# Optimization experiments

Measured on AMD Instinct MI355X. Metric: run time of the kernel, lower is better.

Reference implementation:

```python
import jax, jax.numpy as jnp
import numpy as np

B, S, H = 16, 512, 2048
NH, NKV = 16, 4
HD = H // NH  # 128


def _rope_tables(seq_len, dim, dtype):
    inv_freq = 1.0 / (10000.0 ** (jnp.arange(0, dim, 2, dtype=jnp.float32) / dim))
    t = jnp.arange(seq_len, dtype=jnp.float32)
    freqs = jnp.einsum('i,j->ij', t, inv_freq)          # [S, HD/2]
    emb = jnp.concatenate([freqs, freqs], axis=-1)       # [S, HD]
    cos = jnp.cos(emb)[None, None].astype(dtype)         # [1,1,S,HD]
    sin = jnp.sin(emb)[None, None].astype(dtype)
    return cos, sin


def _rotate_half(x):
    x1, x2 = jnp.split(x, 2, axis=-1)
    return jnp.concatenate([-x2, x1], axis=-1)


def setup_inputs() -> dict:
    key = jax.random.key(0)
    kx, kq, kk, kv, ko = jax.random.split(key, 5)
    x = jax.random.normal(kx, (B, S, H), dtype=jnp.float32)
    s = 0.02
    Wq = jax.random.normal(kq, (H, H), dtype=jnp.float32) * s
    Wk = jax.random.normal(kk, (NKV * HD, H), dtype=jnp.float32) * s
    Wv = jax.random.normal(kv, (NKV * HD, H), dtype=jnp.float32) * s
    Wo = jax.random.normal(ko, (H, H), dtype=jnp.float32) * s
    return {"x": x, "Wq": Wq, "Wk": Wk, "Wv": Wv, "Wo": Wo}


def reference(x, Wq, Wk, Wv, Wo):
    b, s, _ = x.shape
    scaling = HD ** -0.5
    # projections (torch Linear: y = x @ W.T, W is [out,in])
    q = jnp.einsum('bsh,oh->bso', x, Wq).reshape(b, s, NH, HD).transpose(0, 2, 1, 3)
    k = jnp.einsum('bsh,oh->bso', x, Wk).reshape(b, s, NKV, HD).transpose(0, 2, 1, 3)
    v = jnp.einsum('bsh,oh->bso', x, Wv).reshape(b, s, NKV, HD).transpose(0, 2, 1, 3)
    cos, sin = _rope_tables(s, HD, x.dtype)
    q = q * cos + _rotate_half(q) * sin
    k = k * cos + _rotate_half(k) * sin
    rep = NH // NKV
    k = jnp.repeat(k, rep, axis=1)  # [b, NH, s, HD]
    v = jnp.repeat(v, rep, axis=1)
    scores = jnp.einsum('bhqd,bhkd->bhqk', q, k) * scaling
    attn = jax.nn.softmax(scores, axis=-1)
    out = jnp.einsum('bhqk,bhkd->bhqd', attn, v)
    out = out.transpose(0, 2, 1, 3).reshape(b, s, H)
    return jnp.einsum('bsh,oh->bso', out, Wo)
```

## Files before the change

### kernel.cpp

```cpp
#include <hip/hip_runtime.h>
#include <stdint.h>


typedef _Float16 f16;
typedef _Float16 f16x4 __attribute__((ext_vector_type(4)));
typedef _Float16 f16x8 __attribute__((ext_vector_type(8)));
typedef float f32x4 __attribute__((ext_vector_type(4)));

#define B_   16
#define S_   512
#define H_   2048
#define NH_  16
#define NKV_ 4
#define HD_  128
#define ATT_SCALE 0.08838834764831843f
#define LOG2_10000_DIV64 0.20762050593045952f

#define AS1 __attribute__((address_space(1)))
#define AS3 __attribute__((address_space(3)))

__device__ __forceinline__ void async16(const void* g, const void* l) {
  __builtin_amdgcn_global_load_lds((const AS1 unsigned int*)(uintptr_t)g,
                                   (AS3 unsigned int*)(uintptr_t)l, 16, 0, 0);
}

__global__ __launch_bounds__(256) void cast_f32_f16(const float* __restrict__ src,
                                                    f16* __restrict__ dst, int n4) {
  int i = blockIdx.x * 256 + threadIdx.x;
  if (i < n4) {
    float4 v = reinterpret_cast<const float4*>(src)[i];
    f16x4 o = {(f16)v.x, (f16)v.y, (f16)v.z, (f16)v.w};
    reinterpret_cast<f16x4*>(dst)[i] = o;
  }
}

__global__ __launch_bounds__(256) void gemm_qkv(const f16* __restrict__ A,
                                                const f16* __restrict__ W,
                                                f16* __restrict__ qo,
                                                f16* __restrict__ ko,
                                                f16* __restrict__ vto) {
  __shared__ __align__(16) f16 As[128 * 32];
  __shared__ __align__(16) f16 Bs[128 * 32];
  const int K = 2048;
  const int m0 = blockIdx.x * 128;
  const int n0 = blockIdx.y * 128;
  const int tid = threadIdx.x;
  const int wave = tid >> 6, lane = tid & 63;
  const int quad = lane >> 4, l15 = lane & 15;
  const int c0 = wave * 128 + lane;
  const int row0 = c0 >> 2, kc0 = c0 & 3;
  const int row1 = (c0 + 64) >> 2, kc1 = (c0 + 64) & 3;

  f32x4 acc[2][8] = {};

  for (int k0 = 0; k0 < K; k0 += 32) {
    async16(A + (size_t)(m0 + row0) * K + k0 + kc0 * 8, (const char*)As + (wave * 128) * 16);
    async16(A + (size_t)(m0 + row1) * K + k0 + kc1 * 8, (const char*)As + (wave * 128 + 64) * 16);
    async16(W + (size_t)(n0 + row0) * K + k0 + kc0 * 8, (const char*)Bs + (wave * 128) * 16);
    async16(W + (size_t)(n0 + row1) * K + k0 + kc1 * 8, (const char*)Bs + (wave * 128 + 64) * 16);
    __syncthreads();
    f16x8 a[2], b[8];
#pragma unroll
    for (int mi = 0; mi < 2; ++mi)
      a[mi] = *reinterpret_cast<const f16x8*>(As + (wave * 32 + mi * 16 + l15) * 32 + quad * 8);
#pragma unroll
    for (int ni = 0; ni < 8; ++ni)
      b[ni] = *reinterpret_cast<const f16x8*>(Bs + (ni * 16 + l15) * 32 + quad * 8);
#pragma unroll
    for (int mi = 0; mi < 2; ++mi)
#pragma unroll
      for (int ni = 0; ni < 8; ++ni)
        acc[mi][ni] = __builtin_amdgcn_mfma_f32_16x16x32_f16(a[mi], b[ni], acc[mi][ni], 0, 0, 0);
    __syncthreads();
  }

  const int b_ = m0 >> 9;
  if (n0 >= 2560) {
    const int h = (n0 - 2560) >> 7;
    f16* vb = vto + ((size_t)b_ * NKV_ + h) * HD_ * S_;
#pragma unroll
    for (int mi = 0; mi < 2; ++mi)
#pragma unroll
      for (int r = 0; r < 4; ++r) {
        const int s = (m0 + wave * 32 + mi * 16 + quad * 4 + r) & 511;
#pragma unroll
        for (int ni = 0; ni < 8; ++ni) {
          const int d = ni * 16 + l15;
          vb[(size_t)d * S_ + s] = (f16)acc[mi][ni][r];
        }
      }
  } else {
    f16* ob = (n0 < 2048) ? (qo + ((size_t)b_ * NH_ + (n0 >> 7)) * S_ * HD_)
                          : (ko + ((size_t)b_ * NKV_ + ((n0 - 2048) >> 7)) * S_ * HD_);
    float invf[4];
#pragma unroll
    for (int ni = 0; ni < 4; ++ni)
      invf[ni] = exp2f((float)(ni * 16 + l15) * -LOG2_10000_DIV64);
#pragma unroll
    for (int mi = 0; mi < 2; ++mi)
#pragma unroll
      for (int r = 0; r < 4; ++r) {
        const int s = (m0 + wave * 32 + mi * 16 + quad * 4 + r) & 511;
        const size_t rb = (size_t)s * HD_;
#pragma unroll
        for (int ni = 0; ni < 4; ++ni) {
          const int d = ni * 16 + l15;
          float sn, cs;
          __sincosf((float)s * invf[ni], &sn, &cs);
          const float x1 = acc[mi][ni][r], x2 = acc[mi][ni + 4][r];
          ob[rb + d] = (f16)(x1 * cs - x2 * sn);
          ob[rb + d + 64] = (f16)(x2 * cs + x1 * sn);
        }
      }
  }
}

__global__ __launch_bounds__(512) void attn_kernel(const f16* __restrict__ q,
                                                   const f16* __restrict__ k,
                                                   const f16* __restrict__ vt,
                                                   f16* __restrict__ out) {
  __shared__ __align__(16) f16 Qs[128 * 128];
  __shared__ __align__(16) f16 Ks[128 * 128];
  __shared__ __align__(16) f16 Vs[128 * 128];
  __shared__ __align__(16) f16 Ps[8][16 * 136];

  const int qt = blockIdx.x, h = blockIdx.y, b = blockIdx.z;
  const int kvh = h >> 2;
  const int tid = threadIdx.x;
  const int wave = tid >> 6, lane = tid & 63;
  const int quad = lane >> 4, l15 = lane & 15;
  const int sm0 = wave * 16;

  const f16* qbase = q + (((size_t)b * NH_ + h) * S_ + qt * 128) * HD_;
  const f16* kbase = k + ((size_t)b * NKV_ + kvh) * S_ * HD_;
  const f16* vbase = vt + ((size_t)b * NKV_ + kvh) * HD_ * S_;

#pragma unroll
  for (int i = 0; i < 4; ++i) {
    const int L = wave * 256 + i * 64 + lane;
    const int r = L >> 4;
    const int c = (L & 15) ^ (r & 15);
    async16(qbase + (size_t)r * HD_ + c * 8, (const char*)Qs + (size_t)(wave * 256 + i * 64) * 16);
  }

  f32x4 O[8] = {};
  float mrun[4], lrun[4];
#pragma unroll
  for (int r = 0; r < 4; ++r) { mrun[r] = -3.0e38f; lrun[r] = 0.f; }

  for (int j = 0; j < 4; ++j) {
    if (j) __syncthreads();
#pragma unroll
    for (int i = 0; i < 4; ++i) {
      const int L = wave * 256 + i * 64 + lane;
      const int r = L >> 4;
      const int c = (L & 15) ^ (r & 15);
      async16(kbase + (size_t)(j * 128 + r) * HD_ + c * 8,
              (const char*)Ks + (size_t)(wave * 256 + i * 64) * 16);
      async16(vbase + (size_t)r * S_ + j * 128 + c * 8,
              (const char*)Vs + (size_t)(wave * 256 + i * 64) * 16);
    }
    __syncthreads();

    f32x4 Sc[8] = {};
#pragma unroll
    for (int ks = 0; ks < 4; ++ks) {
      f16x8 aq, bk[8];
      aq = *reinterpret_cast<const f16x8*>(Qs + ((sm0 + l15) * 16 + (((ks * 4 + quad) ^ l15))) * 8);
#pragma unroll
      for (int ni = 0; ni < 8; ++ni)
        bk[ni] = *reinterpret_cast<const f16x8*>(Ks + ((ni * 16 + l15) * 16 + ((ks * 4 + quad) ^ l15)) * 8);
#pragma unroll
      for (int ni = 0; ni < 8; ++ni)
        Sc[ni] = __builtin_amdgcn_mfma_f32_16x16x32_f16(aq, bk[ni], Sc[ni], 0, 0, 0);
    }

#pragma unroll
    for (int r = 0; r < 4; ++r) {
      float mx = -3.0e38f;
#pragma unroll
      for (int ni = 0; ni < 8; ++ni) mx = fmaxf(mx, Sc[ni][r]);
      mx *= ATT_SCALE;
#pragma unroll
      for (int off = 1; off < 16; off <<= 1) mx = fmaxf(mx, __shfl_xor(mx, off));
      const float mnew = fmaxf(mrun[r], mx);
      const float alpha = __expf(mrun[r] - mnew);
      float rs = 0.f;
#pragma unroll
      for (int ni = 0; ni < 8; ++ni) {
        const float pv = __expf(Sc[ni][r] * ATT_SCALE - mnew);
        Sc[ni][r] = pv;
        rs += pv;
      }
#pragma unroll
      for (int off = 1; off < 16; off <<= 1) rs += __shfl_xor(rs, off);
      lrun[r] = lrun[r] * alpha + rs;
      mrun[r] = mnew;
#pragma unroll
      for (int ni = 0; ni < 8; ++ni) O[ni][r] *= alpha;
#pragma unroll
      for (int ni = 0; ni < 8; ++ni)
        Ps[wave][(quad * 4 + r) * 136 + ni * 16 + l15] = (f16)Sc[ni][r];
    }

#pragma unroll
    for (int ks = 0; ks < 4; ++ks) {
      f16x8 ap, bv[8];
      ap = *reinterpret_cast<const f16x8*>(&Ps[wave][l15 * 136 + ks * 32 + quad * 8]);
#pragma unroll
      for (int ni = 0; ni < 8; ++ni)
        bv[ni] = *reinterpret_cast<const f16x8*>(Vs + ((ni * 16 + l15) * 16 + ((ks * 4 + quad) ^ l15)) * 8);
#pragma unroll
      for (int ni = 0; ni < 8; ++ni)
        O[ni] = __builtin_amdgcn_mfma_f32_16x16x32_f16(ap, bv[ni], O[ni], 0, 0, 0);
    }
  }

#pragma unroll
  for (int r = 0; r < 4; ++r) {
    const float inv = 1.f / lrun[r];
    const int srow = qt * 128 + sm0 + quad * 4 + r;
#pragma unroll
    for (int ni = 0; ni < 8; ++ni)
      out[((size_t)b * S_ + srow) * H_ + h * HD_ + ni * 16 + l15] = (f16)(O[ni][r] * inv);
  }
}

__global__ __launch_bounds__(256) void gemm_out(const f16* __restrict__ A,
                                                const f16* __restrict__ W,
                                                float* __restrict__ out) {
  __shared__ __align__(16) f16 As[128 * 32];
  __shared__ __align__(16) f16 Bs[128 * 32];
  const int K = 2048;
  const int m0 = blockIdx.x * 128;
  const int n0 = blockIdx.y * 128;
  const int tid = threadIdx.x;
  const int wave = tid >> 6, lane = tid & 63;
  const int quad = lane >> 4, l15 = lane & 15;
  const int wm = wave >> 1, wn = wave & 1;
  const int c0 = wave * 128 + lane;
  const int row0 = c0 >> 2, kc0 = c0 & 3;
  const int row1 = (c0 + 64) >> 2, kc1 = (c0 + 64) & 3;

  f32x4 acc[4][4] = {};

  for (int k0 = 0; k0 < K; k0 += 32) {
    async16(A + (size_t)(m0 + row0) * K + k0 + kc0 * 8, (const char*)As + (wave * 128) * 16);
    async16(A + (size_t)(m0 + row1) * K + k0 + kc1 * 8, (const char*)As + (wave * 128 + 64) * 16);
    async16(W + (size_t)(n0 + row0) * K + k0 + kc0 * 8, (const char*)Bs + (wave * 128) * 16);
    async16(W + (size_t)(n0 + row1) * K + k0 + kc1 * 8, (const char*)Bs + (wave * 128 + 64) * 16);
    __syncthreads();
    f16x8 a[4], b[4];
#pragma unroll
    for (int mi = 0; mi < 4; ++mi)
      a[mi] = *reinterpret_cast<const f16x8*>(As + (wm * 64 + mi * 16 + l15) * 32 + quad * 8);
#pragma unroll
    for (int ni = 0; ni < 4; ++ni)
      b[ni] = *reinterpret_cast<const f16x8*>(Bs + (wn * 64 + ni * 16 + l15) * 32 + quad * 8);
#pragma unroll
    for (int mi = 0; mi < 4; ++mi)
#pragma unroll
      for (int ni = 0; ni < 4; ++ni)
        acc[mi][ni] = __builtin_amdgcn_mfma_f32_16x16x32_f16(a[mi], b[ni], acc[mi][ni], 0, 0, 0);
    __syncthreads();
  }

#pragma unroll
  for (int mi = 0; mi < 4; ++mi) {
#pragma unroll
    for (int ni = 0; ni < 4; ++ni) {
      const int ncol = n0 + wn * 64 + ni * 16 + l15;
#pragma unroll
      for (int r = 0; r < 4; ++r) {
        const int mrow = m0 + wm * 64 + mi * 16 + quad * 4 + r;
        out[(size_t)mrow * 2048 + ncol] = acc[mi][ni][r];
      }
    }
  }
}

extern "C" void kernel_launch(void* const* d_in, const int* in_sizes, int n_in,
                              void* d_out, int out_size, void* d_ws, size_t ws_size,
                              hipStream_t stream) {
  const float* x = (const float*)d_in[0];
  const float* Wq = (const float*)d_in[1];
  const float* Wk = (const float*)d_in[2];
  const float* Wv = (const float*)d_in[3];
  const float* Wo = (const float*)d_in[4];
  float* out = (float*)d_out;
  char* ws = (char*)d_ws;

  f16* x_h  = (f16*)(ws + 0);
  f16* w_h  = (f16*)(ws + 33554432);
  f16* wo_h = (f16*)(ws + 46137344);
  f16* qb   = (f16*)(ws + 54525952);
  f16* kb   = (f16*)(ws + 88080384);
  f16* vtb  = (f16*)(ws + 96468992);
  f16* attn = (f16*)(ws + 104857600);

  cast_f32_f16<<<16384, 256, 0, stream>>>(x, x_h, 4194304);
  cast_f32_f16<<<4096, 256, 0, stream>>>(Wq, w_h, 1048576);
  cast_f32_f16<<<1024, 256, 0, stream>>>(Wk, w_h + 2048 * 2048, 262144);
  cast_f32_f16<<<1024, 256, 0, stream>>>(Wv, w_h + 2560 * 2048, 262144);
  cast_f32_f16<<<4096, 256, 0, stream>>>(Wo, wo_h, 1048576);

  gemm_qkv<<<dim3(64, 24), 256, 0, stream>>>(x_h, w_h, qb, kb, vtb);
  attn_kernel<<<dim3(4, 16, 16), 512, 0, stream>>>(qb, kb, vtb, attn);
  gemm_out<<<dim3(64, 16), 256, 0, stream>>>(attn, wo_h, out);
}
```

Before: 449.4 us.

## Swizzle GEMM LDS tiles, use 2x2 wave tiling in QKV GEMM, fuse casts

Applies an XOR swizzle to the 16-byte chunks of the LDS A/B tiles in both GEMMs, so the fragment reads that feed MFMA hit fewer bank conflicts. The QKV GEMM moves from a 1x4 to a 2x2 wave layout (4x4 MFMA tiles per wave), which balances A/B fragment reuse; the RoPE pairing is remapped so each wave still holds both halves of each rotation pair. The five cast launches are merged into one kernel to cut launch overhead. The swizzle is applied on the global source address side, so correctness depends on reading with the same mapping.

```diff
diff --git a/kernel.cpp b/kernel.cpp
--- a/kernel.cpp
+++ b/kernel.cpp
@@ -24,15 +24,38 @@
                                    (AS3 unsigned int*)(uintptr_t)l, 16, 0, 0);
 }
 
-__global__ __launch_bounds__(256) void cast_f32_f16(const float* __restrict__ src,
-                                                    f16* __restrict__ dst, int n4) {
-  int i = blockIdx.x * 256 + threadIdx.x;
-  if (i < n4) {
-    float4 v = reinterpret_cast<const float4*>(src)[i];
-    f16x4 o = {(f16)v.x, (f16)v.y, (f16)v.z, (f16)v.w};
-    reinterpret_cast<f16x4*>(dst)[i] = o;
-  }
-}
+__global__ __launch_bounds__(256) void cast_all(const float* __restrict__ x,
+                                                const float* __restrict__ wq,
+                                                const float* __restrict__ wk,
+                                                const float* __restrict__ wv,
+                                                const float* __restrict__ wo,
+                                                f16* __restrict__ x_h,
+                                                f16* __restrict__ w_h,
+                                                f16* __restrict__ wo_h) {
+  const int i = blockIdx.x * 256 + threadIdx.x;
+  const float4* src;
+  f16x4* dst;
+  if (i < 4194304) {
+    src = (const float4*)x + i;            dst = (f16x4*)x_h + i;
+  } else if (i < 5242880) {
+    int j = i - 4194304;
+    src = (const float4*)wq + j;           dst = (f16x4*)w_h + j;
+  } else if (i < 5505024) {
+    int j = i - 5242880;
+    src = (const float4*)wk + j;           dst = (f16x4*)w_h + 1048576 + j;
+  } else if (i < 5767168) {
+    int j = i - 5505024;
+    src = (const float4*)wv + j;           dst = (f16x4*)w_h + 1310720 + j;
+  } else {
+    int j = i - 5767168;
+    src = (const float4*)wo + j;           dst = (f16x4*)wo_h + j;
+  }
+  float4 v = *src;
+  f16x4 o = {(f16)v.x, (f16)v.y, (f16)v.z, (f16)v.w};
+  *dst = o;
+}
+
+__device__ __forceinline__ int swz(int r, int c) { return c ^ ((r >> 1) & 3); }
 
 __global__ __launch_bounds__(256) void gemm_qkv(const f16* __restrict__ A,
                                                 const f16* __restrict__ W,
@@ -47,29 +70,34 @@
   const int tid = threadIdx.x;
   const int wave = tid >> 6, lane = tid & 63;
   const int quad = lane >> 4, l15 = lane & 15;
-  const int c0 = wave * 128 + lane;
-  const int row0 = c0 >> 2, kc0 = c0 & 3;
-  const int row1 = (c0 + 64) >> 2, kc1 = (c0 + 64) & 3;
-
-  f32x4 acc[2][8] = {};
+  const int wm = wave >> 1, wn = wave & 1;
+  const int G0 = wave * 128 + lane;
+  const int r0 = G0 >> 2, c0g = swz(r0, G0 & 3);
+  const int r1 = (G0 + 64) >> 2, c1g = swz(r1, (G0 + 64) & 3);
+
+  f32x4 acc[4][4] = {};
 
   for (int k0 = 0; k0 < K; k0 += 32) {
-    async16(A + (size_t)(m0 + row0) * K + k0 + kc0 * 8, (const char*)As + (wave * 128) * 16);
-    async16(A + (size_t)(m0 + row1) * K + k0 + kc1 * 8, (const char*)As + (wave * 128 + 64) * 16);
-    async16(W + (size_t)(n0 + row0) * K + k0 + kc0 * 8, (const char*)Bs + (wave * 128) * 16);
-    async16(W + (size_t)(n0 + row1) * K + k0 + kc1 * 8, (const char*)Bs + (wave * 128 + 64) * 16);
-    __syncthreads();
-    f16x8 a[2], b[8];
-#pragma unroll
-    for (int mi = 0; mi < 2; ++mi)
-      a[mi] = *reinterpret_cast<const f16x8*>(As + (wave * 32 + mi * 16 + l15) * 32 + quad * 8);
-#pragma unroll
-    for (int ni = 0; ni < 8; ++ni)
-      b[ni] = *reinterpret_cast<const f16x8*>(Bs + (ni * 16 + l15) * 32 + quad * 8);
-#pragma unroll
-    for (int mi = 0; mi < 2; ++mi)
-#pragma unroll
-      for (int ni = 0; ni < 8; ++ni)
+    async16(A + (size_t)(m0 + r0) * K + k0 + c0g * 8, (const char*)As + (size_t)G0 * 16);
+    async16(A + (size_t)(m0 + r1) * K + k0 + c1g * 8, (const char*)As + (size_t)(G0 + 64) * 16);
+    async16(W + (size_t)(n0 + r0) * K + k0 + c0g * 8, (const char*)Bs + (size_t)G0 * 16);
+    async16(W + (size_t)(n0 + r1) * K + k0 + c1g * 8, (const char*)Bs + (size_t)(G0 + 64) * 16);
+    __syncthreads();
+    f16x8 a[4], b[4];
+#pragma unroll
+    for (int mi = 0; mi < 4; ++mi) {
+      const int row = wm * 64 + mi * 16 + l15;
+      a[mi] = *reinterpret_cast<const f16x8*>(As + row * 32 + swz(row, quad) * 8);
+    }
+#pragma unroll
+    for (int ni = 0; ni < 4; ++ni) {
+      const int col = (ni >> 1) * 64 + wn * 32 + (ni & 1) * 16 + l15;
+      b[ni] = *reinterpret_cast<const f16x8*>(Bs + col * 32 + swz(col, quad) * 8);
+    }
+#pragma unroll
+    for (int mi = 0; mi < 4; ++mi)
+#pragma unroll
+      for (int ni = 0; ni < 4; ++ni)
         acc[mi][ni] = __builtin_amdgcn_mfma_f32_16x16x32_f16(a[mi], b[ni], acc[mi][ni], 0, 0, 0);
     __syncthreads();
   }
@@ -79,35 +107,35 @@
     const int h = (n0 - 2560) >> 7;
     f16* vb = vto + ((size_t)b_ * NKV_ + h) * HD_ * S_;
 #pragma unroll
-    for (int mi = 0; mi < 2; ++mi)
+    for (int mi = 0; mi < 4; ++mi)
 #pragma unroll
       for (int r = 0; r < 4; ++r) {
-        const int s = (m0 + wave * 32 + mi * 16 + quad * 4 + r) & 511;
-#pragma unroll
-        for (int ni = 0; ni < 8; ++ni) {
-          const int d = ni * 16 + l15;
+        const int s = (m0 + wm * 64 + mi * 16 + quad * 4 + r) & 511;
+#pragma unroll
+        for (int ni = 0; ni < 4; ++ni) {
+          const int d = (ni >> 1) * 64 + wn * 32 + (ni & 1) * 16 + l15;
           vb[(size_t)d * S_ + s] = (f16)acc[mi][ni][r];
         }
       }
   } else {
     f16* ob = (n0 < 2048) ? (qo + ((size_t)b_ * NH_ + (n0 >> 7)) * S_ * HD_)
                           : (ko + ((size_t)b_ * NKV_ + ((n0 - 2048) >> 7)) * S_ * HD_);
-    float invf[4];
-#pragma unroll
-    for (int ni = 0; ni < 4; ++ni)
-      invf[ni] = exp2f((float)(ni * 16 + l15) * -LOG2_10000_DIV64);
-#pragma unroll
-    for (int mi = 0; mi < 2; ++mi)
+    float invf[2];
+#pragma unroll
+    for (int ni = 0; ni < 2; ++ni)
+      invf[ni] = exp2f((float)(wn * 32 + ni * 16 + l15) * -LOG2_10000_DIV64);
+#pragma unroll
+    for (int mi = 0; mi < 4; ++mi)
 #pragma unroll
       for (int r = 0; r < 4; ++r) {
-        const int s = (m0 + wave * 32 + mi * 16 + quad * 4 + r) & 511;
+        const int s = (m0 + wm * 64 + mi * 16 + quad * 4 + r) & 511;
         const size_t rb = (size_t)s * HD_;
 #pragma unroll
-        for (int ni = 0; ni < 4; ++ni) {
-          const int d = ni * 16 + l15;
+        for (int ni = 0; ni < 2; ++ni) {
+          const int d = wn * 32 + ni * 16 + l15;
           float sn, cs;
           __sincosf((float)s * invf[ni], &sn, &cs);
-          const float x1 = acc[mi][ni][r], x2 = acc[mi][ni + 4][r];
+          const float x1 = acc[mi][ni][r], x2 = acc[mi][ni + 2][r];
           ob[rb + d] = (f16)(x1 * cs - x2 * sn);
           ob[rb + d + 64] = (f16)(x2 * cs + x1 * sn);
         }
@@ -238,25 +266,29 @@
   const int wave = tid >> 6, lane = tid & 63;
   const int quad = lane >> 4, l15 = lane & 15;
   const int wm = wave >> 1, wn = wave & 1;
-  const int c0 = wave * 128 + lane;
-  const int row0 = c0 >> 2, kc0 = c0 & 3;
-  const int row1 = (c0 + 64) >> 2, kc1 = (c0 + 64) & 3;
+  const int G0 = wave * 128 + lane;
+  const int r0 = G0 >> 2, c0g = swz(r0, G0 & 3);
+  const int r1 = (G0 + 64) >> 2, c1g = swz(r1, (G0 + 64) & 3);
 
   f32x4 acc[4][4] = {};
 
   for (int k0 = 0; k0 < K; k0 += 32) {
-    async16(A + (size_t)(m0 + row0) * K + k0 + kc0 * 8, (const char*)As + (wave * 128) * 16);
-    async16(A + (size_t)(m0 + row1) * K + k0 + kc1 * 8, (const char*)As + (wave * 128 + 64) * 16);
-    async16(W + (size_t)(n0 + row0) * K + k0 + kc0 * 8, (const char*)Bs + (wave * 128) * 16);
-    async16(W + (size_t)(n0 + row1) * K + k0 + kc1 * 8, (const char*)Bs + (wave * 128 + 64) * 16);
+    async16(A + (size_t)(m0 + r0) * K + k0 + c0g * 8, (const char*)As + (size_t)G0 * 16);
+    async16(A + (size_t)(m0 + r1) * K + k0 + c1g * 8, (const char*)As + (size_t)(G0 + 64) * 16);
+    async16(W + (size_t)(n0 + r0) * K + k0 + c0g * 8, (const char*)Bs + (size_t)G0 * 16);
+    async16(W + (size_t)(n0 + r1) * K + k0 + c1g * 8, (const char*)Bs + (size_t)(G0 + 64) * 16);
     __syncthreads();
     f16x8 a[4], b[4];
 #pragma unroll
-    for (int mi = 0; mi < 4; ++mi)
-      a[mi] = *reinterpret_cast<const f16x8*>(As + (wm * 64 + mi * 16 + l15) * 32 + quad * 8);
-#pragma unroll
-    for (int ni = 0; ni < 4; ++ni)
-      b[ni] = *reinterpret_cast<const f16x8*>(Bs + (wn * 64 + ni * 16 + l15) * 32 + quad * 8);
+    for (int mi = 0; mi < 4; ++mi) {
+      const int row = wm * 64 + mi * 16 + l15;
+      a[mi] = *reinterpret_cast<const f16x8*>(As + row * 32 + swz(row, quad) * 8);
+    }
+#pragma unroll
+    for (int ni = 0; ni < 4; ++ni) {
+      const int col = wn * 64 + ni * 16 + l15;
+      b[ni] = *reinterpret_cast<const f16x8*>(Bs + col * 32 + swz(col, quad) * 8);
+    }
 #pragma unroll
     for (int mi = 0; mi < 4; ++mi)
 #pragma unroll
@@ -298,12 +330,7 @@
   f16* vtb  = (f16*)(ws + 96468992);
   f16* attn = (f16*)(ws + 104857600);
 
-  cast_f32_f16<<<16384, 256, 0, stream>>>(x, x_h, 4194304);
-  cast_f32_f16<<<4096, 256, 0, stream>>>(Wq, w_h, 1048576);
-  cast_f32_f16<<<1024, 256, 0, stream>>>(Wk, w_h + 2048 * 2048, 262144);
-  cast_f32_f16<<<1024, 256, 0, stream>>>(Wv, w_h + 2560 * 2048, 262144);
-  cast_f32_f16<<<4096, 256, 0, stream>>>(Wo, wo_h, 1048576);
-
+  cast_all<<<26624, 256, 0, stream>>>(x, Wq, Wk, Wv, Wo, x_h, w_h, wo_h);
   gemm_qkv<<<dim3(64, 24), 256, 0, stream>>>(x_h, w_h, qb, kb, vtb);
   attn_kernel<<<dim3(4, 16, 16), 512, 0, stream>>>(qb, kb, vtb, attn);
   gemm_out<<<dim3(64, 16), 256, 0, stream>>>(attn, wo_h, out);
```

After: 444.4 us. About the same (-1.1%).
